# Kernel optimization log

Measured on AMD Instinct MI355X. Metric: run time of the kernel, lower is better.

## Reference

```python
import jax, jax.numpy as jnp
import numpy as np

B = 16          # graphs per batch (equal-sized, contiguous)
N_PER = 16384   # nodes per graph
N = B * N_PER   # 262144 total nodes
E = 524288      # total edges
D_IN = 128
D_OUT = 128
RATIO = 0.5
K = int(N_PER * RATIO)  # nodes kept per graph by TopKPooling
NEG_SLOPE = 0.01        # F.leaky_relu default


def setup_inputs() -> dict:
    key = jax.random.key(0)
    ks = jax.random.split(key, 7)
    x = jax.random.normal(ks[0], (N, D_IN), jnp.float32)
    # edges constrained within each graph so per-graph pooling is meaningful
    e_per = E // B
    off = (jnp.arange(B, dtype=jnp.int32) * N_PER)[:, None]
    src = jax.random.randint(ks[1], (B, e_per), 0, N_PER, dtype=jnp.int32) + off
    dst = jax.random.randint(ks[2], (B, e_per), 0, N_PER, dtype=jnp.int32) + off
    edge_index = jnp.stack([src.reshape(-1), dst.reshape(-1)], axis=0)
    edge_weight = jax.random.uniform(ks[3], (E,), jnp.float32)
    batch = jnp.repeat(jnp.arange(B, dtype=jnp.int32), N_PER)
    conv_weight = jax.random.normal(ks[4], (D_IN, D_OUT), jnp.float32) / np.sqrt(D_IN)
    conv_bias = jnp.zeros((D_OUT,), jnp.float32)
    pool_weight = jax.random.normal(ks[5], (D_OUT,), jnp.float32)
    return {"x": x, "edge_index": edge_index, "edge_weight": edge_weight,
            "batch": batch, "conv_weight": conv_weight, "conv_bias": conv_bias,
            "pool_weight": pool_weight}


def reference(x, edge_index, edge_weight, batch, conv_weight, conv_bias, pool_weight):
    # Dropout is identity in eval mode (p=0.0).
    row, col = edge_index[0], edge_index[1]

    # ---- GCNConv: gcn_norm with added self-loops (fill_value=1) ----
    loop = jnp.arange(N, dtype=row.dtype)
    row_sl = jnp.concatenate([row, loop])
    col_sl = jnp.concatenate([col, loop])
    w_sl = jnp.concatenate([edge_weight, jnp.ones((N,), edge_weight.dtype)])
    deg = jax.ops.segment_sum(w_sl, col_sl, num_segments=N)          # in-degree at targets
    dinv = jnp.where(deg > 0, jax.lax.rsqrt(deg), 0.0)
    norm = dinv[row_sl] * w_sl * dinv[col_sl]                        # [E+N]

    xw = x @ conv_weight                                             # [N, D_OUT]
    msgs = norm[:, None] * xw[row_sl]                                # gather at sources
    h = jax.ops.segment_sum(msgs, col_sl, num_segments=N) + conv_bias  # scatter-add at targets
    h = jax.nn.leaky_relu(h, NEG_SLOPE)

    # ---- TopKPooling: score = tanh(x . w / ||w||), keep top K per graph ----
    score = jnp.tanh((h @ pool_weight) / jnp.linalg.norm(pool_weight))  # [N]
    _, idx = jax.lax.top_k(score.reshape(B, N_PER), K)                  # [B, K] local idx
    perm = (idx + (jnp.arange(B, dtype=idx.dtype) * N_PER)[:, None]).reshape(-1)  # [B*K]

    x_out = h[perm] * score[perm][:, None]                              # gate kept nodes
    batch_new = batch[perm]

    # ---- filter_adj: relabel, keep edges whose both endpoints survive ----
    mapping = jnp.full((N,), -1, dtype=row.dtype).at[perm].set(
        jnp.arange(B * K, dtype=row.dtype))
    r2, c2 = mapping[row], mapping[col]
    valid = (r2 >= 0) & (c2 >= 0)
    edge_index_new = jnp.where(valid, jnp.stack([r2, c2], axis=0), 0)   # padded (static shape)
    edge_weight_new = jnp.where(valid, edge_weight, 0.0)
    return x_out, edge_index_new, edge_weight_new, batch_new
```

## Files before the change

kernel.cpp:

```cpp
#include <hip/hip_runtime.h>
#include <math.h>

#define N_NODES 262144
#define N_EDGES 524288
#define NB      16
#define N_PER   16384
#define KKEEP   8192
#define DIM     128
#define NEG_SLOPE 0.01f
#define CHUNK   2048

#define X_OUT   0
#define X_EI    16777216
#define X_EW    17825792
#define X_BATCH 18350080

__device__ __forceinline__ unsigned long long pack_key(float sc, int localIdx) {
    unsigned int u = __float_as_uint(sc);
    u = (u & 0x80000000u) ? ~u : (u | 0x80000000u);
    unsigned int inv = ~u;
    return ((unsigned long long)inv << 32) | (unsigned int)localIdx;
}

__global__ void k_init(float* deg, int* count, int* mapping, const float* pw, float* normPw) {
    int n = blockIdx.x * 256 + threadIdx.x;
    if (n < N_NODES) { deg[n] = 1.0f; count[n] = 0; mapping[n] = -1; }
    if (n == 0) {
        float s = 0.f;
        for (int i = 0; i < DIM; i++) s += pw[i] * pw[i];
        normPw[0] = sqrtf(s);
    }
}

__global__ void k_deg(const int* col, const float* w, float* deg, int* count) {
    int e = blockIdx.x * 256 + threadIdx.x;
    if (e >= N_EDGES) return;
    int c = col[e];
    atomicAdd(&deg[c], w[e]);
    atomicAdd(&count[c], 1);
}

__global__ void k_scan1(const int* count, int* offs, int* blockSums) {
    __shared__ int s[2048];
    int base = blockIdx.x * 2048;
    int t = threadIdx.x;
    s[t]        = count[base + t];
    s[t + 1024] = count[base + t + 1024];
    __syncthreads();
    for (int off = 1; off < 2048; off <<= 1) {
        int a0 = (t >= off)        ? s[t - off]        : 0;
        int a1 = (t + 1024 >= off) ? s[t + 1024 - off] : 0;
        __syncthreads();
        s[t]        += a0;
        s[t + 1024] += a1;
        __syncthreads();
    }
    offs[base + t]        = s[t]        - count[base + t];
    offs[base + t + 1024] = s[t + 1024] - count[base + t + 1024];
    if (t == 0) blockSums[blockIdx.x] = s[2047];
}

__global__ void k_scan2(int* blockSums, int* offs) {
    if (threadIdx.x == 0) {
        int run = 0;
        for (int b = 0; b < 128; b++) { int v = blockSums[b]; blockSums[b] = run; run += v; }
        offs[N_NODES] = run;
    }
}

__global__ void k_fixup(int* offs, int* count, float* deg, const int* blockSums) {
    int n = blockIdx.x * 256 + threadIdx.x;
    if (n >= N_NODES) return;
    offs[n] += blockSums[n >> 11];
    count[n] = 0;
    float d = deg[n];
    deg[n] = (d > 0.f) ? (1.0f / sqrtf(d)) : 0.f;
}

__global__ void k_scatter(const int* row, const int* col, const float* w, const float* dinv,
                          const int* offs, int* cursor, int* ssrc, float* scoef) {
    int e = blockIdx.x * 256 + threadIdx.x;
    if (e >= N_EDGES) return;
    int r = row[e], c = col[e];
    int pos = atomicAdd(&cursor[c], 1);
    int slot = offs[c] + pos;
    ssrc[slot]  = r;
    scoef[slot] = (dinv[r] * w[e]) * dinv[c];
}

__global__ void k_aggregate(const float* x, const float* dinv, const int* offs,
                            const int* ssrc, const float* scoef, float* agg) {
    int g = blockIdx.x * 256 + threadIdx.x;
    int node = g >> 5, d = g & 31;
    const float4* x4 = (const float4*)x;
    float4 acc = make_float4(0.f, 0.f, 0.f, 0.f);
    int s = offs[node], e = offs[node + 1];
    for (int j = s; j < e; j++) {
        int   src = ssrc[j];
        float cf  = scoef[j];
        float4 v = x4[(size_t)src * 32 + d];
        acc.x += cf * v.x; acc.y += cf * v.y; acc.z += cf * v.z; acc.w += cf * v.w;
    }
    float di = dinv[node];
    float cf = di * di;
    float4 v = x4[(size_t)node * 32 + d];
    acc.x += cf * v.x; acc.y += cf * v.y; acc.z += cf * v.z; acc.w += cf * v.w;
    ((float4*)agg)[(size_t)node * 32 + d] = acc;
}

__global__ __launch_bounds__(256, 2) void k_gemm(float* hio, const float* Wg,
                                                 const float* bias, const float* pw,
                                                 const float* normPw, float* score) {
    __shared__ __align__(16) float sW[32 * 128];
    __shared__ __align__(16) float sA[32 * 128];
    int tid = threadIdx.x;
    int cx = tid & 15;
    int ry = tid >> 4;
    int row0 = blockIdx.x * 128;

    float acc[8][8];
#pragma unroll
    for (int r = 0; r < 8; r++)
#pragma unroll
        for (int c = 0; c < 8; c++) acc[r][c] = 0.f;

    for (int k0 = 0; k0 < DIM; k0 += 32) {
#pragma unroll
        for (int i = 0; i < 4; i++) {
            int f = tid + i * 256;
            int kk = f >> 5, j4 = f & 31;
            *(float4*)(sW + kk * 128 + j4 * 4) =
                *(const float4*)(Wg + (size_t)(k0 + kk) * 128 + j4 * 4);
        }
#pragma unroll
        for (int i = 0; i < 4; i++) {
            int f = tid + i * 256;
            int r = f >> 3, k4 = f & 7;
            float4 v = *(const float4*)(hio + (size_t)(row0 + r) * 128 + k0 + k4 * 4);
            int rs = r ^ (k4 * 8);
            sA[(k4 * 4 + 0) * 128 + rs] = v.x;
            sA[(k4 * 4 + 1) * 128 + rs] = v.y;
            sA[(k4 * 4 + 2) * 128 + rs] = v.z;
            sA[(k4 * 4 + 3) * 128 + rs] = v.w;
        }
        __syncthreads();
#pragma unroll
        for (int kk = 0; kk < 32; kk++) {
            const float* ap = sA + kk * 128 + ((8 * ry) ^ ((kk >> 2) * 8));
            float4 a0 = *(const float4*)(ap);
            float4 a1 = *(const float4*)(ap + 4);
            float4 w0 = *(const float4*)(sW + kk * 128 + 8 * cx);
            float4 w1 = *(const float4*)(sW + kk * 128 + 8 * cx + 4);
            float av[8] = {a0.x, a0.y, a0.z, a0.w, a1.x, a1.y, a1.z, a1.w};
            float wv[8] = {w0.x, w0.y, w0.z, w0.w, w1.x, w1.y, w1.z, w1.w};
#pragma unroll
            for (int r = 0; r < 8; r++)
#pragma unroll
                for (int c = 0; c < 8; c++) acc[r][c] += av[r] * wv[c];
        }
        __syncthreads();
    }

    float bv[8], pv[8];
#pragma unroll
    for (int c = 0; c < 8; c++) { bv[c] = bias[8 * cx + c]; pv[c] = pw[8 * cx + c]; }
    float nrm = normPw[0];

#pragma unroll
    for (int r = 0; r < 8; r++) {
        int row = row0 + 8 * ry + r;
        float hv[8];
        float p = 0.f;
#pragma unroll
        for (int c = 0; c < 8; c++) {
            float v = acc[r][c] + bv[c];
            v = (v >= 0.f) ? v : NEG_SLOPE * v;
            hv[c] = v;
            p += v * pv[c];
        }
        float4 o0 = make_float4(hv[0], hv[1], hv[2], hv[3]);
        float4 o1 = make_float4(hv[4], hv[5], hv[6], hv[7]);
        *(float4*)(hio + (size_t)row * 128 + 8 * cx)     = o0;
        *(float4*)(hio + (size_t)row * 128 + 8 * cx + 4) = o1;
#pragma unroll
        for (int m = 1; m < 16; m <<= 1) p += __shfl_xor(p, m, 64);
        if (cx == 0) score[row] = tanhf(p / nrm);
    }
}

__global__ void __launch_bounds__(1024) k_sortchunks(const float* score,
                                                     unsigned long long* keys) {
    __shared__ unsigned long long a[CHUNK];
    int base = blockIdx.x * CHUNK;
    int t = threadIdx.x;
#pragma unroll
    for (int i = 0; i < CHUNK / 1024; i++) {
        int p = t + i * 1024;
        int node = base + p;
        a[p] = pack_key(score[node], node & (N_PER - 1));
    }
    __syncthreads();
    for (int k = 2; k <= CHUNK; k <<= 1) {
        for (int j = k >> 1; j > 0; j >>= 1) {
#pragma unroll
            for (int q = 0; q < CHUNK / 2048; q++) {
                int tt = t + q * 1024;
                int i = ((tt & ~(j - 1)) << 1) | (tt & (j - 1));
                int l = i | j;
                bool asc = ((i & k) == 0);
                unsigned long long x = a[i], y = a[l];
                if ((x > y) == asc) { a[i] = y; a[l] = x; }
            }
            __syncthreads();
        }
    }
#pragma unroll
    for (int i = 0; i < CHUNK / 1024; i++) {
        int p = t + i * 1024;
        keys[base + p] = a[p];
    }
}

__global__ void k_rank(const float* score, const unsigned long long* keys,
                       int* perm, int* mapping, float* out) {
    int n = blockIdx.x * 256 + threadIdx.x;
    if (n >= N_NODES) return;
    int g = n >> 14;
    unsigned long long key = pack_key(score[n], n & (N_PER - 1));
    const unsigned long long* gb = keys + ((size_t)g << 14);
    int r = 0;
#pragma unroll
    for (int c = 0; c < N_PER / CHUNK; c++) {
        const unsigned long long* ch = gb + c * CHUNK;
        int lo = 0, hi = CHUNK;
        while (lo < hi) {
            int mid = (lo + hi) >> 1;
            if (ch[mid] < key) lo = mid + 1; else hi = mid;
        }
        r += lo;
    }
    if (r < KKEEP) {
        int i = (g << 13) + r;
        perm[i] = n;
        mapping[n] = i;
        out[X_BATCH + i] = (float)g;
    }
}

__global__ void k_gate(const float* h, const float* score, const int* perm, float* out) {
    int g = blockIdx.x * 256 + threadIdx.x;
    int i = g >> 5, d = g & 31;
    int node = perm[i];
    float sc = score[node];
    float4 v = ((const float4*)h)[(size_t)node * 32 + d];
    v.x *= sc; v.y *= sc; v.z *= sc; v.w *= sc;
    ((float4*)(out + X_OUT))[(size_t)i * 32 + d] = v;
}

__global__ void k_edges(const int* row, const int* col, const float* w,
                        const int* mapping, float* out) {
    int e = blockIdx.x * 256 + threadIdx.x;
    if (e >= N_EDGES) return;
    int mr = mapping[row[e]], mc = mapping[col[e]];
    bool valid = (mr >= 0) && (mc >= 0);
    out[X_EI + e]           = valid ? (float)mr : 0.f;
    out[X_EI + N_EDGES + e] = valid ? (float)mc : 0.f;
    out[X_EW + e]           = valid ? w[e] : 0.f;
}

extern "C" void kernel_launch(void* const* d_in, const int* in_sizes, int n_in,
                              void* d_out, int out_size, void* d_ws, size_t ws_size,
                              hipStream_t stream) {
    const float* x     = (const float*)d_in[0];
    const int*   ei    = (const int*)d_in[1];
    const float* ew    = (const float*)d_in[2];
    const float* Wc    = (const float*)d_in[4];
    const float* bias  = (const float*)d_in[5];
    const float* pw    = (const float*)d_in[6];
    float* out = (float*)d_out;

    const int* rowp = ei;
    const int* colp = ei + N_EDGES;

    char* wsb = (char*)d_ws;
    float* agg     = (float*)(wsb);
    float* dinv    = (float*)(wsb + 134217728);
    int*   count   = (int*)  (wsb + 135266304);
    int*   offs    = (int*)  (wsb + 136314880);
    int*   ssrc    = (int*)  (wsb + 137363712);
    float* scoef   = (float*)(wsb + 139460864);
    float* score   = (float*)(wsb + 141557760);
    unsigned long long* keys = (unsigned long long*)(wsb + 142606336);
    int*   perm    = (int*)  (wsb + 144703488);
    int*   mapping = (int*)  (wsb + 145227776);
    int*   blockSums = (int*)(wsb + 146276352);
    float* normPw  = (float*)(wsb + 146277376);

    k_init   <<<N_NODES / 256, 256, 0, stream>>>(dinv, count, mapping, pw, normPw);
    k_deg    <<<N_EDGES / 256, 256, 0, stream>>>(colp, ew, dinv, count);
    k_scan1  <<<128, 1024, 0, stream>>>(count, offs, blockSums);
    k_scan2  <<<1, 64, 0, stream>>>(blockSums, offs);
    k_fixup  <<<N_NODES / 256, 256, 0, stream>>>(offs, count, dinv, blockSums);
    k_scatter<<<N_EDGES / 256, 256, 0, stream>>>(rowp, colp, ew, dinv, offs, count, ssrc, scoef);
    k_aggregate<<<(N_NODES * 32) / 256, 256, 0, stream>>>(x, dinv, offs, ssrc, scoef, agg);
    k_gemm   <<<N_NODES / 128, 256, 0, stream>>>(agg, Wc, bias, pw, normPw, score);
    k_sortchunks<<<N_NODES / CHUNK, 1024, 0, stream>>>(score, keys);
    k_rank   <<<N_NODES / 256, 256, 0, stream>>>(score, keys, perm, mapping, out);
    k_gate   <<<(NB * KKEEP * 32) / 256, 256, 0, stream>>>(agg, score, perm, out);
    k_edges  <<<N_EDGES / 256, 256, 0, stream>>>(rowp, colp, ew, mapping, out);
}
```

Baseline: 550.0 us.

## Replace FP32 SIMT GEMM with split-bf16 MFMA emulation of fp32

```diff
diff --git a/kernel.cpp b/kernel.cpp
--- a/kernel.cpp
+++ b/kernel.cpp
@@ -15,12 +15,21 @@
 #define X_EW    17825792
 #define X_BATCH 18350080
 
+typedef short s8v __attribute__((ext_vector_type(8)));
+typedef float f4v __attribute__((ext_vector_type(4)));
+
 __device__ __forceinline__ unsigned long long pack_key(float sc, int localIdx) {
     unsigned int u = __float_as_uint(sc);
     u = (u & 0x80000000u) ? ~u : (u | 0x80000000u);
     unsigned int inv = ~u;
     return ((unsigned long long)inv << 32) | (unsigned int)localIdx;
 }
+
+__device__ __forceinline__ unsigned int f2bf(float x) {
+    unsigned int u = __float_as_uint(x);
+    return (u + 0x7FFFu + ((u >> 16) & 1u)) >> 16;
+}
+__device__ __forceinline__ float bf2f(unsigned int h) { return __uint_as_float(h << 16); }
 
 __global__ void k_init(float* deg, int* count, int* mapping, const float* pw, float* normPw) {
     int n = blockIdx.x * 256 + threadIdx.x;
@@ -29,6 +38,24 @@
         float s = 0.f;
         for (int i = 0; i < DIM; i++) s += pw[i] * pw[i];
         normPw[0] = sqrtf(s);
+    }
+}
+
+__global__ void k_wprep(const float* Wg, unsigned short* Wt0, unsigned short* Wt1,
+                        unsigned short* Wt2) {
+    int tid = threadIdx.x;
+    for (int j = 0; j < 64; j++) {
+        int idx = tid + j * 256;
+        int k = idx >> 7, n = idx & 127;
+        float wv = Wg[k * 128 + n];
+        unsigned int h = f2bf(wv);
+        float r1 = wv - bf2f(h);
+        unsigned int m = f2bf(r1);
+        float r2 = r1 - bf2f(m);
+        unsigned int lo = f2bf(r2);
+        Wt0[n * 128 + k] = (unsigned short)h;
+        Wt1[n * 128 + k] = (unsigned short)m;
+        Wt2[n * 128 + k] = (unsigned short)lo;
     }
 }
 
@@ -108,83 +135,145 @@
     ((float4*)agg)[(size_t)node * 32 + d] = acc;
 }
 
-__global__ __launch_bounds__(256, 2) void k_gemm(float* hio, const float* Wg,
+__global__ __launch_bounds__(256, 2) void k_gemm(float* hio,
+                                                 const unsigned short* Wt0,
+                                                 const unsigned short* Wt1,
+                                                 const unsigned short* Wt2,
                                                  const float* bias, const float* pw,
                                                  const float* normPw, float* score) {
-    __shared__ __align__(16) float sW[32 * 128];
-    __shared__ __align__(16) float sA[32 * 128];
+    __shared__ __align__(16) char smem[49152];
+    char* sA0 = smem;
+    char* sA1 = smem + 8192;
+    char* sA2 = smem + 16384;
+    char* sW0 = smem + 24576;
+    char* sW1 = smem + 32768;
+    char* sW2 = smem + 40960;
+
     int tid = threadIdx.x;
-    int cx = tid & 15;
-    int ry = tid >> 4;
+    int l   = tid & 63;
+    int w   = tid >> 6;
+    int l15 = l & 15, l4 = l >> 4;
     int row0 = blockIdx.x * 128;
 
-    float acc[8][8];
-#pragma unroll
-    for (int r = 0; r < 8; r++)
-#pragma unroll
-        for (int c = 0; c < 8; c++) acc[r][c] = 0.f;
-
-    for (int k0 = 0; k0 < DIM; k0 += 32) {
-#pragma unroll
-        for (int i = 0; i < 4; i++) {
+    f4v acc[2][8];
+#pragma unroll
+    for (int mt = 0; mt < 2; mt++)
+#pragma unroll
+        for (int nt = 0; nt < 8; nt++)
+#pragma unroll
+            for (int r = 0; r < 4; r++) acc[mt][nt][r] = 0.f;
+
+    for (int kh = 0; kh < 4; kh++) {
+        if (kh) __syncthreads();
+#pragma unroll
+        for (int i = 0; i < 2; i++) {
             int f = tid + i * 256;
-            int kk = f >> 5, j4 = f & 31;
-            *(float4*)(sW + kk * 128 + j4 * 4) =
-                *(const float4*)(Wg + (size_t)(k0 + kk) * 128 + j4 * 4);
-        }
-#pragma unroll
-        for (int i = 0; i < 4; i++) {
+            int r = f >> 2, c = f & 3;
+            const float* src = hio + (size_t)(row0 + r) * 128 + kh * 32 + c * 8;
+            float4 v0 = *(const float4*)(src);
+            float4 v1 = *(const float4*)(src + 4);
+            float a[8] = {v0.x, v0.y, v0.z, v0.w, v1.x, v1.y, v1.z, v1.w};
+            unsigned int h[8], m[8], lo[8];
+#pragma unroll
+            for (int j = 0; j < 8; j++) {
+                h[j] = f2bf(a[j]);
+                float r1 = a[j] - bf2f(h[j]);
+                m[j] = f2bf(r1);
+                float r2 = r1 - bf2f(m[j]);
+                lo[j] = f2bf(r2);
+            }
+            int off = r * 64 + ((c ^ ((r >> 1) & 3)) * 16);
+            *(uint4*)(sA0 + off) = make_uint4(h[0] | (h[1] << 16), h[2] | (h[3] << 16),
+                                              h[4] | (h[5] << 16), h[6] | (h[7] << 16));
+            *(uint4*)(sA1 + off) = make_uint4(m[0] | (m[1] << 16), m[2] | (m[3] << 16),
+                                              m[4] | (m[5] << 16), m[6] | (m[7] << 16));
+            *(uint4*)(sA2 + off) = make_uint4(lo[0] | (lo[1] << 16), lo[2] | (lo[3] << 16),
+                                              lo[4] | (lo[5] << 16), lo[6] | (lo[7] << 16));
+        }
+#pragma unroll
+        for (int i = 0; i < 2; i++) {
             int f = tid + i * 256;
-            int r = f >> 3, k4 = f & 7;
-            float4 v = *(const float4*)(hio + (size_t)(row0 + r) * 128 + k0 + k4 * 4);
-            int rs = r ^ (k4 * 8);
-            sA[(k4 * 4 + 0) * 128 + rs] = v.x;
-            sA[(k4 * 4 + 1) * 128 + rs] = v.y;
-            sA[(k4 * 4 + 2) * 128 + rs] = v.z;
-            sA[(k4 * 4 + 3) * 128 + rs] = v.w;
+            int n = f >> 2, c = f & 3;
+            size_t gb = (size_t)n * 256 + kh * 64 + c * 16;
+            int off = n * 64 + ((c ^ ((n >> 1) & 3)) * 16);
+            *(uint4*)(sW0 + off) = *(const uint4*)((const char*)Wt0 + gb);
+            *(uint4*)(sW1 + off) = *(const uint4*)((const char*)Wt1 + gb);
+            *(uint4*)(sW2 + off) = *(const uint4*)((const char*)Wt2 + gb);
         }
         __syncthreads();
-#pragma unroll
-        for (int kk = 0; kk < 32; kk++) {
-            const float* ap = sA + kk * 128 + ((8 * ry) ^ ((kk >> 2) * 8));
-            float4 a0 = *(const float4*)(ap);
-            float4 a1 = *(const float4*)(ap + 4);
-            float4 w0 = *(const float4*)(sW + kk * 128 + 8 * cx);
-            float4 w1 = *(const float4*)(sW + kk * 128 + 8 * cx + 4);
-            float av[8] = {a0.x, a0.y, a0.z, a0.w, a1.x, a1.y, a1.z, a1.w};
-            float wv[8] = {w0.x, w0.y, w0.z, w0.w, w1.x, w1.y, w1.z, w1.w};
-#pragma unroll
-            for (int r = 0; r < 8; r++)
-#pragma unroll
-                for (int c = 0; c < 8; c++) acc[r][c] += av[r] * wv[c];
-        }
-        __syncthreads();
+
+        s8v ah[2], am[2], al[2];
+#pragma unroll
+        for (int mt = 0; mt < 2; mt++) {
+            int r = w * 32 + mt * 16 + l15;
+            int off = r * 64 + ((l4 ^ ((r >> 1) & 3)) * 16);
+            ah[mt] = *(const s8v*)(sA0 + off);
+            am[mt] = *(const s8v*)(sA1 + off);
+            al[mt] = *(const s8v*)(sA2 + off);
+        }
+#pragma unroll
+        for (int nt = 0; nt < 8; nt++) {
+            int rn = nt * 16 + l15;
+            int offb = rn * 64 + ((l4 ^ ((rn >> 1) & 3)) * 16);
+            s8v b0 = *(const s8v*)(sW0 + offb);
+            s8v b1 = *(const s8v*)(sW1 + offb);
+            s8v b2 = *(const s8v*)(sW2 + offb);
+#pragma unroll
+            for (int mt = 0; mt < 2; mt++) {
+                acc[mt][nt] = __builtin_amdgcn_mfma_f32_16x16x32_bf16(ah[mt], b0, acc[mt][nt], 0, 0, 0);
+                acc[mt][nt] = __builtin_amdgcn_mfma_f32_16x16x32_bf16(ah[mt], b1, acc[mt][nt], 0, 0, 0);
+                acc[mt][nt] = __builtin_amdgcn_mfma_f32_16x16x32_bf16(am[mt], b0, acc[mt][nt], 0, 0, 0);
+                acc[mt][nt] = __builtin_amdgcn_mfma_f32_16x16x32_bf16(am[mt], b1, acc[mt][nt], 0, 0, 0);
+                acc[mt][nt] = __builtin_amdgcn_mfma_f32_16x16x32_bf16(ah[mt], b2, acc[mt][nt], 0, 0, 0);
+                acc[mt][nt] = __builtin_amdgcn_mfma_f32_16x16x32_bf16(al[mt], b0, acc[mt][nt], 0, 0, 0);
+                acc[mt][nt] = __builtin_amdgcn_mfma_f32_16x16x32_bf16(am[mt], b2, acc[mt][nt], 0, 0, 0);
+                acc[mt][nt] = __builtin_amdgcn_mfma_f32_16x16x32_bf16(al[mt], b1, acc[mt][nt], 0, 0, 0);
+            }
+        }
     }
 
     float bv[8], pv[8];
 #pragma unroll
-    for (int c = 0; c < 8; c++) { bv[c] = bias[8 * cx + c]; pv[c] = pw[8 * cx + c]; }
+    for (int nt = 0; nt < 8; nt++) {
+        bv[nt] = bias[nt * 16 + l15];
+        pv[nt] = pw[nt * 16 + l15];
+    }
     float nrm = normPw[0];
-
-#pragma unroll
-    for (int r = 0; r < 8; r++) {
-        int row = row0 + 8 * ry + r;
-        float hv[8];
-        float p = 0.f;
-#pragma unroll
-        for (int c = 0; c < 8; c++) {
-            float v = acc[r][c] + bv[c];
-            v = (v >= 0.f) ? v : NEG_SLOPE * v;
-            hv[c] = v;
-            p += v * pv[c];
-        }
-        float4 o0 = make_float4(hv[0], hv[1], hv[2], hv[3]);
-        float4 o1 = make_float4(hv[4], hv[5], hv[6], hv[7]);
-        *(float4*)(hio + (size_t)row * 128 + 8 * cx)     = o0;
-        *(float4*)(hio + (size_t)row * 128 + 8 * cx + 4) = o1;
-#pragma unroll
-        for (int m = 1; m < 16; m <<= 1) p += __shfl_xor(p, m, 64);
-        if (cx == 0) score[row] = tanhf(p / nrm);
+    float sp[2][4];
+#pragma unroll
+    for (int mt = 0; mt < 2; mt++)
+#pragma unroll
+        for (int r = 0; r < 4; r++) sp[mt][r] = 0.f;
+
+#pragma unroll
+    for (int mt = 0; mt < 2; mt++) {
+#pragma unroll
+        for (int r = 0; r < 4; r++) {
+            int row = row0 + w * 32 + mt * 16 + l4 * 4 + r;
+#pragma unroll
+            for (int nt = 0; nt < 8; nt++) {
+                float v = acc[mt][nt][r] + bv[nt];
+                v = (v >= 0.f) ? v : NEG_SLOPE * v;
+                hio[(size_t)row * 128 + nt * 16 + l15] = v;
+                sp[mt][r] += v * pv[nt];
+            }
+        }
+    }
+#pragma unroll
+    for (int m = 1; m < 16; m <<= 1) {
+#pragma unroll
+        for (int mt = 0; mt < 2; mt++)
+#pragma unroll
+            for (int r = 0; r < 4; r++) sp[mt][r] += __shfl_xor(sp[mt][r], m, 64);
+    }
+    if (l15 == 0) {
+#pragma unroll
+        for (int mt = 0; mt < 2; mt++)
+#pragma unroll
+            for (int r = 0; r < 4; r++) {
+                int row = row0 + w * 32 + mt * 16 + l4 * 4 + r;
+                score[row] = tanhf(sp[mt][r] / nrm);
+            }
     }
 }
 
@@ -295,15 +384,19 @@
     int*   mapping = (int*)  (wsb + 145227776);
     int*   blockSums = (int*)(wsb + 146276352);
     float* normPw  = (float*)(wsb + 146277376);
+    unsigned short* Wt0 = (unsigned short*)(wsb + 146278400);
+    unsigned short* Wt1 = (unsigned short*)(wsb + 146311168);
+    unsigned short* Wt2 = (unsigned short*)(wsb + 146343936);
 
     k_init   <<<N_NODES / 256, 256, 0, stream>>>(dinv, count, mapping, pw, normPw);
+    k_wprep  <<<1, 256, 0, stream>>>(Wc, Wt0, Wt1, Wt2);
     k_deg    <<<N_EDGES / 256, 256, 0, stream>>>(colp, ew, dinv, count);
     k_scan1  <<<128, 1024, 0, stream>>>(count, offs, blockSums);
     k_scan2  <<<1, 64, 0, stream>>>(blockSums, offs);
     k_fixup  <<<N_NODES / 256, 256, 0, stream>>>(offs, count, dinv, blockSums);
     k_scatter<<<N_EDGES / 256, 256, 0, stream>>>(rowp, colp, ew, dinv, offs, count, ssrc, scoef);
     k_aggregate<<<(N_NODES * 32) / 256, 256, 0, stream>>>(x, dinv, offs, ssrc, scoef, agg);
-    k_gemm   <<<N_NODES / 128, 256, 0, stream>>>(agg, Wc, bias, pw, normPw, score);
+    k_gemm   <<<N_NODES / 128, 256, 0, stream>>>(agg, Wt0, Wt1, Wt2, bias, pw, normPw, score);
     k_sortchunks<<<N_NODES / CHUNK, 1024, 0, stream>>>(score, keys);
     k_rank   <<<N_NODES / 256, 256, 0, stream>>>(score, keys, perm, mapping, out);
     k_gate   <<<(NB * KKEEP * 32) / 256, 256, 0, stream>>>(agg, score, perm, out);
```

New measurement: 580.4 us. 5.5% more time.
